# Performance work log

Hardware: AMD Instinct MI355X
Metric: run time of the kernel (lower is better)

## Reference

```python
import jax, jax.numpy as jnp
import numpy as np

SCALE = 0.08838834764831845  # 1/sqrt(128)


def setup_inputs() -> dict:
    key = jax.random.key(0)
    k1, k2, k3, k4 = jax.random.split(key, 4)
    B, Sq, H, D = 1, 2048, 32, 128
    Skv, K = 4096, 256
    return {
        "q": jax.random.normal(k1, (B, Sq, H, D), jnp.float32),
        "kv": jax.random.normal(k2, (B, Skv, 2, D), jnp.float32),  # stacked K,V (MQA)
        "attn_sink": jax.random.normal(k3, (H,), jnp.float32),
        "topk_idxs": jax.random.randint(k4, (B, Sq, K), 0, Skv),
    }


def reference(q, kv, attn_sink, topk_idxs):
    # q:        [B, Sq, H, D]
    # kv:       [B, Skv, 2, D]  (index 0 = keys, 1 = values; shared across heads)
    # topk_idxs:[B, Sq, K]      per-query selected KV positions
    # attn_sink:[H]             per-head sink logit added to the softmax denominator
    B = q.shape[0]
    # Gather selected KV per query: [B, Sq, K, 2, D]
    gathered = kv[jnp.arange(B)[:, None, None], topk_idxs]
    k = gathered[..., 0, :]  # [B, Sq, K, D]
    v = gathered[..., 1, :]  # [B, Sq, K, D]

    scores = jnp.einsum("bqhd,bqkd->bqhk", q, k) * SCALE  # [B, Sq, H, K]
    sink = attn_sink[None, None, :, None]                  # [1, 1, H, 1]

    # Numerically stable softmax over K selected tokens + sink logit.
    m = jnp.maximum(jnp.max(scores, axis=-1, keepdims=True), sink)
    e = jnp.exp(scores - m)
    denom = jnp.sum(e, axis=-1, keepdims=True) + jnp.exp(sink - m)
    probs = e / denom                                      # sink absorbs leftover mass

    out = jnp.einsum("bqhk,bqkd->bqhd", probs, v)          # [B, Sq, H, D]
    return out
```

## Files before the change

### kernel.cpp

```cpp
#include <hip/hip_runtime.h>
#include <hip/hip_bf16.h>

#define SQ 2048
#define NH 32
#define DH 128
#define NK 256
#define SCALE 0.08838834764831845f
#define LOG2E 1.4426950408889634f

typedef __attribute__((ext_vector_type(8))) __bf16 bf16x8;
typedef __attribute__((ext_vector_type(4))) float floatx4;

#define VB_STRIDE 72
#define PB_STRIDE 264

#define OFF_VB   16896
#define OFF_SINK 35328
#define OFF_RED  35456
#define OFF_RED2 35968
#define SMEM_SZ  36480

__device__ __forceinline__ unsigned pk_bf16(float a, float b) {
  union { __hip_bfloat162 h2; unsigned u; } c;
  c.h2 = __float22bfloat162_rn(make_float2(a, b));
  return c.u;
}

__device__ __forceinline__ float fast_exp2(float x) {
#if __has_builtin(__builtin_amdgcn_exp2f)
  return __builtin_amdgcn_exp2f(x);
#else
  return exp2f(x);
#endif
}

template <int CTRL>
__device__ __forceinline__ float dpp_rot(float x) {
  int i = __builtin_bit_cast(int, x);
  i = __builtin_amdgcn_mov_dpp(i, CTRL, 0xF, 0xF, true);
  return __builtin_bit_cast(float, i);
}
#define RED16_MAX(v) { v = fmaxf(v, dpp_rot<0x121>(v)); v = fmaxf(v, dpp_rot<0x122>(v)); \
                       v = fmaxf(v, dpp_rot<0x124>(v)); v = fmaxf(v, dpp_rot<0x128>(v)); }
#define RED16_SUM(v) { v += dpp_rot<0x121>(v); v += dpp_rot<0x122>(v); \
                       v += dpp_rot<0x124>(v); v += dpp_rot<0x128>(v); }

__global__ __launch_bounds__(256) void kv_to_bf16(const float* __restrict__ kv,
                                                  unsigned short* __restrict__ kvb) {
  int i = blockIdx.x * 256 + threadIdx.x;
  float4 f = ((const float4*)kv)[i];
  uint2 o = { pk_bf16(f.x, f.y), pk_bf16(f.z, f.w) };
  ((uint2*)kvb)[i] = o;
}

struct VR { uint4 a, b, c, d; };

__device__ __forceinline__ VR v_load_g(const unsigned short* __restrict__ kvb,
                                       const int* __restrict__ tkg, int c, int tid) {
  int rg = tid & 15, dg = tid >> 4;
  int r0 = rg * 4, d0 = dg * 8;
  int4 i4 = *(const int4*)(tkg + c * 64 + r0);
  VR v;
  v.a = *(const uint4*)(kvb + (size_t)i4.x * 256 + 128 + d0);
  v.b = *(const uint4*)(kvb + (size_t)i4.y * 256 + 128 + d0);
  v.c = *(const uint4*)(kvb + (size_t)i4.z * 256 + 128 + d0);
  v.d = *(const uint4*)(kvb + (size_t)i4.w * 256 + 128 + d0);
  return v;
}

__device__ __forceinline__ void v_write(unsigned short* vbuf, const VR& v, int tid) {
  int rg = tid & 15, dg = tid >> 4;
  int r0 = rg * 4, d0 = dg * 8;
  const unsigned* pa = (const unsigned*)&v.a;
  const unsigned* pb = (const unsigned*)&v.b;
  const unsigned* pc = (const unsigned*)&v.c;
  const unsigned* pd = (const unsigned*)&v.d;
#pragma unroll
  for (int w = 0; w < 4; w++) {
    unsigned lo01 = __builtin_amdgcn_perm(pb[w], pa[w], 0x05040100u);
    unsigned lo23 = __builtin_amdgcn_perm(pd[w], pc[w], 0x05040100u);
    unsigned hi01 = __builtin_amdgcn_perm(pb[w], pa[w], 0x07060302u);
    unsigned hi23 = __builtin_amdgcn_perm(pd[w], pc[w], 0x07060302u);
    uint2 lo = { lo01, lo23 }, hi = { hi01, hi23 };
    *(uint2*)&vbuf[(d0 + 2 * w) * VB_STRIDE + r0] = lo;
    *(uint2*)&vbuf[(d0 + 2 * w + 1) * VB_STRIDE + r0] = hi;
  }
}

__device__ __forceinline__ void pv_chunk(const unsigned short* pbuf,
                                         const unsigned short* vbuf, int c,
                                         int wave, int quad, int l16,
                                         floatx4 oacc[2][2]) {
#pragma unroll
  for (int ks = 0; ks < 2; ks++) {
    int kof = c * 64 + ks * 32 + quad * 8;
    bf16x8 a0 = *(const bf16x8*)&pbuf[l16 * PB_STRIDE + kof];
    bf16x8 a1 = *(const bf16x8*)&pbuf[(16 + l16) * PB_STRIDE + kof];
    int kl = ks * 32 + quad * 8;
    bf16x8 b0 = *(const bf16x8*)&vbuf[(wave * 32 + l16) * VB_STRIDE + kl];
    bf16x8 b1 = *(const bf16x8*)&vbuf[(wave * 32 + 16 + l16) * VB_STRIDE + kl];
    oacc[0][0] = __builtin_amdgcn_mfma_f32_16x16x32_bf16(a0, b0, oacc[0][0], 0, 0, 0);
    oacc[0][1] = __builtin_amdgcn_mfma_f32_16x16x32_bf16(a0, b1, oacc[0][1], 0, 0, 0);
    oacc[1][0] = __builtin_amdgcn_mfma_f32_16x16x32_bf16(a1, b0, oacc[1][0], 0, 0, 0);
    oacc[1][1] = __builtin_amdgcn_mfma_f32_16x16x32_bf16(a1, b1, oacc[1][1], 0, 0, 0);
  }
}

__global__ __launch_bounds__(256, 4) void sparse_attn_kernel(
    const float* __restrict__ q, const unsigned short* __restrict__ kvb,
    const float* __restrict__ sink, const int* __restrict__ topk,
    float* __restrict__ out) {
  __shared__ __align__(16) char smem[SMEM_SZ];
  unsigned short* pbuf = (unsigned short*)smem;
  unsigned short* vbuf = (unsigned short*)(smem + OFF_VB);
  float* sink_s = (float*)(smem + OFF_SINK);
  float* red    = (float*)(smem + OFF_RED);
  float* red2   = (float*)(smem + OFF_RED2);

  const int tid = threadIdx.x;
  const int s = blockIdx.x;
  const int wave = tid >> 6;
  const int lane = tid & 63;
  const int quad = lane >> 4;
  const int l16 = lane & 15;
  const int* tkg = topk + (size_t)s * NK;
  const float QSC = SCALE * LOG2E;

  if (tid < 32) sink_s[tid] = sink[tid] * LOG2E;

  int kidx[4];
#pragma unroll
  for (int c = 0; c < 4; c++) kidx[c] = tkg[c * 64 + wave * 16 + l16];

  bf16x8 afrag[2][4];
#pragma unroll
  for (int mt = 0; mt < 2; mt++)
#pragma unroll
    for (int ks = 0; ks < 4; ks++) {
      const float4* p = (const float4*)(q + (size_t)s * (NH * DH) +
                                        (mt * 16 + l16) * DH + ks * 32 + quad * 8);
      float4 f0 = p[0], f1 = p[1];
      union { uint4 u; bf16x8 h; } cv;
      cv.u = (uint4){ pk_bf16(f0.x, f0.y), pk_bf16(f0.z, f0.w),
                      pk_bf16(f1.x, f1.y), pk_bf16(f1.z, f1.w) };
      afrag[mt][ks] = cv.h;
    }

  floatx4 sc[4][2];
  bf16x8 bk[2][4];
#pragma unroll
  for (int ks = 0; ks < 4; ks++)
    bk[0][ks] = *(const bf16x8*)(kvb + (size_t)kidx[0] * 256 + ks * 32 + quad * 8);
#pragma unroll
  for (int c = 0; c < 4; c++) {
    if (c < 3) {
#pragma unroll
      for (int ks = 0; ks < 4; ks++)
        bk[(c + 1) & 1][ks] =
            *(const bf16x8*)(kvb + (size_t)kidx[c + 1] * 256 + ks * 32 + quad * 8);
    }
    floatx4 a0 = {0.f, 0.f, 0.f, 0.f};
    floatx4 a1 = {0.f, 0.f, 0.f, 0.f};
#pragma unroll
    for (int ks = 0; ks < 4; ks++) {
      a0 = __builtin_amdgcn_mfma_f32_16x16x32_bf16(afrag[0][ks], bk[c & 1][ks], a0, 0, 0, 0);
      a1 = __builtin_amdgcn_mfma_f32_16x16x32_bf16(afrag[1][ks], bk[c & 1][ks], a1, 0, 0, 0);
    }
    sc[c][0] = a0;
    sc[c][1] = a1;
  }

  VR v0 = v_load_g(kvb, tkg, 0, tid);

  float mh[2][4];
#pragma unroll
  for (int mt = 0; mt < 2; mt++)
#pragma unroll
    for (int r = 0; r < 4; r++) {
      float v = fmaxf(fmaxf(sc[0][mt][r], sc[1][mt][r]),
                      fmaxf(sc[2][mt][r], sc[3][mt][r]));
      RED16_MAX(v);
      mh[mt][r] = v;
    }
  if (l16 == 0) {
#pragma unroll
    for (int mt = 0; mt < 2; mt++)
#pragma unroll
      for (int r = 0; r < 4; r++)
        red[wave * 32 + mt * 16 + quad * 4 + r] = mh[mt][r];
  }
  __syncthreads();
  v_write(vbuf, v0, tid);
  VR v1 = v_load_g(kvb, tkg, 1, tid);
#pragma unroll
  for (int mt = 0; mt < 2; mt++)
#pragma unroll
    for (int r = 0; r < 4; r++) {
      int h = mt * 16 + quad * 4 + r;
      float v = red[h];
#pragma unroll
      for (int w = 1; w < 4; w++) v = fmaxf(v, red[w * 32 + h]);
      mh[mt][r] = fmaxf(v * QSC, sink_s[h]);
    }
  float ps[2][4];
#pragma unroll
  for (int mt = 0; mt < 2; mt++)
#pragma unroll
    for (int r = 0; r < 4; r++) {
      float acc = 0.f;
#pragma unroll
      for (int c = 0; c < 4; c++) {
        float e = fast_exp2(fmaf(sc[c][mt][r], QSC, -mh[mt][r]));
        sc[c][mt][r] = e;
        acc += e;
      }
      RED16_SUM(acc);
      ps[mt][r] = acc;
    }
  if (l16 == 0) {
#pragma unroll
    for (int mt = 0; mt < 2; mt++)
#pragma unroll
      for (int r = 0; r < 4; r++)
        red2[wave * 32 + mt * 16 + quad * 4 + r] = ps[mt][r];
  }
  __syncthreads();
  float inv[2][4];
#pragma unroll
  for (int mt = 0; mt < 2; mt++)
#pragma unroll
    for (int r = 0; r < 4; r++) {
      int h = mt * 16 + quad * 4 + r;
      float dd = fast_exp2(sink_s[h] - mh[mt][r]);
#pragma unroll
      for (int w = 0; w < 4; w++) dd += red2[w * 32 + h];
      inv[mt][r] = 1.0f / dd;
    }
#pragma unroll
  for (int c = 0; c < 4; c++)
#pragma unroll
    for (int mt = 0; mt < 2; mt++) {
      int col = c * 64 + wave * 16 + l16;
      unsigned short* pb = &pbuf[(mt * 16 + quad * 4) * PB_STRIDE + col];
      unsigned p01 = pk_bf16(sc[c][mt][0], sc[c][mt][1]);
      unsigned p23 = pk_bf16(sc[c][mt][2], sc[c][mt][3]);
      pb[0] = (unsigned short)p01;
      pb[PB_STRIDE] = (unsigned short)(p01 >> 16);
      pb[2 * PB_STRIDE] = (unsigned short)p23;
      pb[3 * PB_STRIDE] = (unsigned short)(p23 >> 16);
    }
  __syncthreads();

  floatx4 oacc[2][2];
#pragma unroll
  for (int mt = 0; mt < 2; mt++)
#pragma unroll
    for (int nt = 0; nt < 2; nt++)
      oacc[mt][nt] = (floatx4){0.f, 0.f, 0.f, 0.f};

  pv_chunk(pbuf, vbuf, 0, wave, quad, l16, oacc);
  __syncthreads();
  v_write(vbuf, v1, tid);
  VR v2 = v_load_g(kvb, tkg, 2, tid);
  __syncthreads();

  pv_chunk(pbuf, vbuf, 1, wave, quad, l16, oacc);
  __syncthreads();
  v_write(vbuf, v2, tid);
  VR v3 = v_load_g(kvb, tkg, 3, tid);
  __syncthreads();

  pv_chunk(pbuf, vbuf, 2, wave, quad, l16, oacc);
  __syncthreads();
  v_write(vbuf, v3, tid);
  __syncthreads();

  pv_chunk(pbuf, vbuf, 3, wave, quad, l16, oacc);

  {
    float* op = out + (size_t)s * (NH * DH);
#pragma unroll
    for (int mt = 0; mt < 2; mt++)
#pragma unroll
      for (int nt = 0; nt < 2; nt++)
#pragma unroll
        for (int r4 = 0; r4 < 4; r4++) {
          int h = mt * 16 + quad * 4 + r4;
          int d = wave * 32 + nt * 16 + l16;
          op[h * DH + d] = oacc[mt][nt][r4] * inv[mt][r4];
        }
  }
}

extern "C" void kernel_launch(void* const* d_in, const int* in_sizes, int n_in,
                              void* d_out, int out_size, void* d_ws, size_t ws_size,
                              hipStream_t stream) {
  (void)in_sizes; (void)n_in; (void)out_size; (void)ws_size;
  const float* q    = (const float*)d_in[0];
  const float* kv   = (const float*)d_in[1];
  const float* sink = (const float*)d_in[2];
  const int*   topk = (const int*)d_in[3];
  float* out = (float*)d_out;
  unsigned short* kvb = (unsigned short*)d_ws;

  kv_to_bf16<<<dim3(1024), dim3(256), 0, stream>>>(kv, kvb);
  sparse_attn_kernel<<<dim3(SQ), dim3(256), 0, stream>>>(q, kvb, sink, topk, out);
}
```

Before: 130.0 us.

## Use per-wave LDS slots for K and V staging, drop block barriers

Each wave now loads its own 32-column slice of V and K rows into a private LDS slot, so the PV loop needs only compiler memory fences instead of __syncthreads. K rows are loaded as contiguous 64-byte chunks per lane and transposed through LDS before the QK MFMAs, and two V chunks are prefetched at once. The aim is to remove block-wide barrier stalls and make the gathered global loads more coalesced. The cost is extra LDS traffic and registers, and it relies on wave-level ordering of LDS accesses with only compiler fences and no hardware waits.

Result: slower. 167.3 us (+28.7%).

```diff
diff --git a/kernel.cpp b/kernel.cpp
--- a/kernel.cpp
+++ b/kernel.cpp
@@ -11,10 +11,14 @@
 typedef __attribute__((ext_vector_type(8))) __bf16 bf16x8;
 typedef __attribute__((ext_vector_type(4))) float floatx4;
 
+#define LDS_FENCE() asm volatile("" ::: "memory")
+
+#define KS_STRIDE 136
 #define VB_STRIDE 72
 #define PB_STRIDE 264
-
-#define OFF_VB   16896
+#define WSLOT 4608
+
+#define OFF_KV   16896
 #define OFF_SINK 35328
 #define OFF_RED  35456
 #define OFF_RED2 35968
@@ -55,22 +59,21 @@
 
 struct VR { uint4 a, b, c, d; };
 
-__device__ __forceinline__ VR v_load_g(const unsigned short* __restrict__ kvb,
-                                       const int* __restrict__ tkg, int c, int tid) {
-  int rg = tid & 15, dg = tid >> 4;
-  int r0 = rg * 4, d0 = dg * 8;
-  int4 i4 = *(const int4*)(tkg + c * 64 + r0);
+__device__ __forceinline__ VR v_load_w(const unsigned short* __restrict__ kvb,
+                                       const int* __restrict__ tkg, int c,
+                                       int wave, int quad, int l16) {
+  int4 i4 = *(const int4*)(tkg + c * 64 + 4 * l16);
+  int off = 128 + wave * 32 + quad * 8;
   VR v;
-  v.a = *(const uint4*)(kvb + (size_t)i4.x * 256 + 128 + d0);
-  v.b = *(const uint4*)(kvb + (size_t)i4.y * 256 + 128 + d0);
-  v.c = *(const uint4*)(kvb + (size_t)i4.z * 256 + 128 + d0);
-  v.d = *(const uint4*)(kvb + (size_t)i4.w * 256 + 128 + d0);
+  v.a = *(const uint4*)(kvb + (size_t)i4.x * 256 + off);
+  v.b = *(const uint4*)(kvb + (size_t)i4.y * 256 + off);
+  v.c = *(const uint4*)(kvb + (size_t)i4.z * 256 + off);
+  v.d = *(const uint4*)(kvb + (size_t)i4.w * 256 + off);
   return v;
 }
 
-__device__ __forceinline__ void v_write(unsigned short* vbuf, const VR& v, int tid) {
-  int rg = tid & 15, dg = tid >> 4;
-  int r0 = rg * 4, d0 = dg * 8;
+__device__ __forceinline__ void v_write_w(unsigned short* kvw, const VR& v,
+                                          int quad, int l16) {
   const unsigned* pa = (const unsigned*)&v.a;
   const unsigned* pb = (const unsigned*)&v.b;
   const unsigned* pc = (const unsigned*)&v.c;
@@ -82,23 +85,23 @@
     unsigned hi01 = __builtin_amdgcn_perm(pb[w], pa[w], 0x07060302u);
     unsigned hi23 = __builtin_amdgcn_perm(pd[w], pc[w], 0x07060302u);
     uint2 lo = { lo01, lo23 }, hi = { hi01, hi23 };
-    *(uint2*)&vbuf[(d0 + 2 * w) * VB_STRIDE + r0] = lo;
-    *(uint2*)&vbuf[(d0 + 2 * w + 1) * VB_STRIDE + r0] = hi;
+    int dl = quad * 8 + 2 * w;
+    *(uint2*)&kvw[dl * VB_STRIDE + 4 * l16] = lo;
+    *(uint2*)&kvw[(dl + 1) * VB_STRIDE + 4 * l16] = hi;
   }
 }
 
 __device__ __forceinline__ void pv_chunk(const unsigned short* pbuf,
-                                         const unsigned short* vbuf, int c,
-                                         int wave, int quad, int l16,
-                                         floatx4 oacc[2][2]) {
+                                         const unsigned short* kvw, int c,
+                                         int quad, int l16, floatx4 oacc[2][2]) {
 #pragma unroll
   for (int ks = 0; ks < 2; ks++) {
     int kof = c * 64 + ks * 32 + quad * 8;
     bf16x8 a0 = *(const bf16x8*)&pbuf[l16 * PB_STRIDE + kof];
     bf16x8 a1 = *(const bf16x8*)&pbuf[(16 + l16) * PB_STRIDE + kof];
     int kl = ks * 32 + quad * 8;
-    bf16x8 b0 = *(const bf16x8*)&vbuf[(wave * 32 + l16) * VB_STRIDE + kl];
-    bf16x8 b1 = *(const bf16x8*)&vbuf[(wave * 32 + 16 + l16) * VB_STRIDE + kl];
+    bf16x8 b0 = *(const bf16x8*)&kvw[l16 * VB_STRIDE + kl];
+    bf16x8 b1 = *(const bf16x8*)&kvw[(16 + l16) * VB_STRIDE + kl];
     oacc[0][0] = __builtin_amdgcn_mfma_f32_16x16x32_bf16(a0, b0, oacc[0][0], 0, 0, 0);
     oacc[0][1] = __builtin_amdgcn_mfma_f32_16x16x32_bf16(a0, b1, oacc[0][1], 0, 0, 0);
     oacc[1][0] = __builtin_amdgcn_mfma_f32_16x16x32_bf16(a1, b0, oacc[1][0], 0, 0, 0);
@@ -112,7 +115,6 @@
     float* __restrict__ out) {
   __shared__ __align__(16) char smem[SMEM_SZ];
   unsigned short* pbuf = (unsigned short*)smem;
-  unsigned short* vbuf = (unsigned short*)(smem + OFF_VB);
   float* sink_s = (float*)(smem + OFF_SINK);
   float* red    = (float*)(smem + OFF_RED);
   float* red2   = (float*)(smem + OFF_RED2);
@@ -125,6 +127,7 @@
   const int l16 = lane & 15;
   const int* tkg = topk + (size_t)s * NK;
   const float QSC = SCALE * LOG2E;
+  unsigned short* kvw = (unsigned short*)(smem + OFF_KV + wave * WSLOT);
 
   if (tid < 32) sink_s[tid] = sink[tid] * LOG2E;
 
@@ -146,31 +149,45 @@
       afrag[mt][ks] = cv.h;
     }
 
+  uint4 kr0[4], kr1[4];
+#pragma unroll
+  for (int i = 0; i < 4; i++)
+    kr0[i] = *(const uint4*)(kvb + (size_t)kidx[0] * 256 + quad * 32 + i * 8);
+#pragma unroll
+  for (int i = 0; i < 4; i++)
+    kr1[i] = *(const uint4*)(kvb + (size_t)kidx[1] * 256 + quad * 32 + i * 8);
+
   floatx4 sc[4][2];
-  bf16x8 bk[2][4];
-#pragma unroll
-  for (int ks = 0; ks < 4; ks++)
-    bk[0][ks] = *(const bf16x8*)(kvb + (size_t)kidx[0] * 256 + ks * 32 + quad * 8);
 #pragma unroll
   for (int c = 0; c < 4; c++) {
-    if (c < 3) {
-#pragma unroll
-      for (int ks = 0; ks < 4; ks++)
-        bk[(c + 1) & 1][ks] =
-            *(const bf16x8*)(kvb + (size_t)kidx[c + 1] * 256 + ks * 32 + quad * 8);
-    }
+    uint4* kcur = (c & 1) ? kr1 : kr0;
+    LDS_FENCE();
+#pragma unroll
+    for (int i = 0; i < 4; i++)
+      *(uint4*)&kvw[l16 * KS_STRIDE + quad * 32 + i * 8] = kcur[i];
+    if (c + 2 < 4) {
+#pragma unroll
+      for (int i = 0; i < 4; i++)
+        kcur[i] = *(const uint4*)(kvb + (size_t)kidx[c + 2] * 256 + quad * 32 + i * 8);
+    }
+    LDS_FENCE();
+    bf16x8 bfr[4];
+#pragma unroll
+    for (int ks = 0; ks < 4; ks++)
+      bfr[ks] = *(const bf16x8*)&kvw[l16 * KS_STRIDE + ks * 32 + quad * 8];
     floatx4 a0 = {0.f, 0.f, 0.f, 0.f};
     floatx4 a1 = {0.f, 0.f, 0.f, 0.f};
 #pragma unroll
     for (int ks = 0; ks < 4; ks++) {
-      a0 = __builtin_amdgcn_mfma_f32_16x16x32_bf16(afrag[0][ks], bk[c & 1][ks], a0, 0, 0, 0);
-      a1 = __builtin_amdgcn_mfma_f32_16x16x32_bf16(afrag[1][ks], bk[c & 1][ks], a1, 0, 0, 0);
+      a0 = __builtin_amdgcn_mfma_f32_16x16x32_bf16(afrag[0][ks], bfr[ks], a0, 0, 0, 0);
+      a1 = __builtin_amdgcn_mfma_f32_16x16x32_bf16(afrag[1][ks], bfr[ks], a1, 0, 0, 0);
     }
     sc[c][0] = a0;
     sc[c][1] = a1;
   }
 
-  VR v0 = v_load_g(kvb, tkg, 0, tid);
+  VR va = v_load_w(kvb, tkg, 0, wave, quad, l16);
+  VR vb = v_load_w(kvb, tkg, 1, wave, quad, l16);
 
   float mh[2][4];
 #pragma unroll
@@ -190,8 +207,8 @@
         red[wave * 32 + mt * 16 + quad * 4 + r] = mh[mt][r];
   }
   __syncthreads();
-  v_write(vbuf, v0, tid);
-  VR v1 = v_load_g(kvb, tkg, 1, tid);
+  v_write_w(kvw, va, quad, l16);
+  va = v_load_w(kvb, tkg, 2, wave, quad, l16);
 #pragma unroll
   for (int mt = 0; mt < 2; mt++)
 #pragma unroll
@@ -258,24 +275,23 @@
     for (int nt = 0; nt < 2; nt++)
       oacc[mt][nt] = (floatx4){0.f, 0.f, 0.f, 0.f};
 
-  pv_chunk(pbuf, vbuf, 0, wave, quad, l16, oacc);
-  __syncthreads();
-  v_write(vbuf, v1, tid);
-  VR v2 = v_load_g(kvb, tkg, 2, tid);
-  __syncthreads();
-
-  pv_chunk(pbuf, vbuf, 1, wave, quad, l16, oacc);
-  __syncthreads();
-  v_write(vbuf, v2, tid);
-  VR v3 = v_load_g(kvb, tkg, 3, tid);
-  __syncthreads();
-
-  pv_chunk(pbuf, vbuf, 2, wave, quad, l16, oacc);
-  __syncthreads();
-  v_write(vbuf, v3, tid);
-  __syncthreads();
-
-  pv_chunk(pbuf, vbuf, 3, wave, quad, l16, oacc);
+  pv_chunk(pbuf, kvw, 0, quad, l16, oacc);
+  LDS_FENCE();
+  v_write_w(kvw, vb, quad, l16);
+  vb = v_load_w(kvb, tkg, 3, wave, quad, l16);
+  LDS_FENCE();
+
+  pv_chunk(pbuf, kvw, 1, quad, l16, oacc);
+  LDS_FENCE();
+  v_write_w(kvw, va, quad, l16);
+  LDS_FENCE();
+
+  pv_chunk(pbuf, kvw, 2, quad, l16, oacc);
+  LDS_FENCE();
+  v_write_w(kvw, vb, quad, l16);
+  LDS_FENCE();
+
+  pv_chunk(pbuf, kvw, 3, quad, l16, oacc);
 
   {
     float* op = out + (size_t)s * (NH * DH);
```
